# Performance work log

Hardware: AMD Instinct MI355X
Metric: run time of the kernel (lower is better)

Reference implementation:

```python
import jax, jax.numpy as jnp
import numpy as np

N_NODES = 100000
N_EDGES = 1600000
HIDDEN = 128
EF_DIM = 16
LAYERS = 2
N_GRAPHS = 64


def _residual(x, W, b):
    # Residual(mlp_num=2): x + act(act(x@W0+b0)@W1+b1), act = silu
    h = jax.nn.silu(x @ W[0] + b[0])
    h = jax.nn.silu(h @ W[1] + b[1])
    return x + h


def setup_inputs() -> dict:
    key = jax.random.key(0)
    ks = jax.random.split(key, 10)
    scalar = jax.random.normal(ks[0], (N_NODES, HIDDEN), jnp.float32)
    ef = jax.random.normal(ks[1], (N_EDGES, EF_DIM), jnp.float32)
    edge_index = jax.random.randint(ks[2], (2, N_EDGES), 0, N_NODES, jnp.int32)
    C = jax.random.uniform(ks[3], (N_NODES, 1), dtype=jnp.float32)
    conv_smooth = jax.random.uniform(ks[4], (N_EDGES, 1), dtype=jnp.float32)
    batch_index = jnp.sort(jax.random.randint(ks[5], (N_NODES,), 0, N_GRAPHS, jnp.int32))
    # per VD_Conv layer: emb0, emb1, conv0, conv1, out0, out1 residual blocks; + 3 pooling blocks
    n_res = LAYERS * 6 + 3
    res_W = jax.random.normal(ks[6], (n_res, 2, HIDDEN, HIDDEN), jnp.float32) * 0.02
    res_b = jnp.zeros((n_res, 2, HIDDEN), jnp.float32)
    e_lin = jax.random.normal(ks[7], (LAYERS, EF_DIM, HIDDEN), jnp.float32) * 0.02
    return {"scalar": scalar, "ef": ef, "edge_index": edge_index, "C": C,
            "conv_smooth": conv_smooth, "batch_index": batch_index,
            "res_W": res_W, "res_b": res_b, "e_lin": e_lin}


def reference(scalar, ef, edge_index, C, conv_smooth, batch_index, res_W, res_b, e_lin):
    row, col = edge_index[0], edge_index[1]
    for i in range(LAYERS):
        p = 6 * i
        s_src = _residual(scalar, res_W[p], res_b[p])
        s_dst = _residual(scalar, res_W[p + 1], res_b[p + 1])
        conv_filter = (ef @ e_lin[i]) * conv_smooth            # [E, H]
        scalar_edge = s_dst[col] * conv_filter                 # gather + elementwise filter
        conv = jax.ops.segment_sum(scalar_edge, row, num_segments=N_NODES) * C  # scatter-reduce (agg='sum')
        conv = _residual(_residual(conv, res_W[p + 2], res_b[p + 2]), res_W[p + 3], res_b[p + 3])
        s = s_src * conv
        s = _residual(_residual(s, res_W[p + 4], res_b[p + 4]), res_W[p + 5], res_b[p + 5])
        scalar = s + scalar                                    # outer residual in Vanilla_DisGNN
    graph = jax.ops.segment_sum(scalar, batch_index, num_segments=N_GRAPHS)
    q = 6 * LAYERS
    for j in range(3):
        graph = _residual(graph, res_W[q + j], res_b[q + j])
    return graph
```

## Files before the change

### kernel.cpp

```cpp
#include <hip/hip_runtime.h>
#include <hip/hip_bf16.h>
#include <cstdint>
#include <cstddef>

#define HD 128
#define WOFF 32768

typedef __bf16    bf16x8 __attribute__((ext_vector_type(8)));
typedef float     f32x4  __attribute__((ext_vector_type(4)));
typedef _Float16  h2     __attribute__((ext_vector_type(2)));
typedef _Float16  h8     __attribute__((ext_vector_type(8)));

#if defined(__has_builtin)
#if __has_builtin(__builtin_amdgcn_fdot2)
#define HAVE_FDOT2 1
#endif
#endif

__device__ __forceinline__ float fdot2f(h2 a, h2 b, float c) {
#ifdef HAVE_FDOT2
    return __builtin_amdgcn_fdot2(a, b, c, false);
#else
    return c + (float)a[0]*(float)b[0] + (float)a[1]*(float)b[1];
#endif
}

__device__ __forceinline__ int swz(int r, int byteInRow) {
    int chunk = (byteInRow >> 4) ^ (r & 7);
    return r * 256 + (chunk << 4) + (byteInRow & 15);
}

__device__ __forceinline__ float silu_f(float v) { return v / (1.f + __expf(-v)); }


__device__ __forceinline__ void stage_x64(const float* __restrict__ x, char* lds,
                                          int r0, int nrows, int tid) {
    const int q = tid & 15;
    #pragma unroll
    for (int rr = 0; rr < 2; ++rr) {
        const int r  = (tid >> 4) + rr * 32;
        const int gr = r0 + r;
        float4 a = {0,0,0,0}, b = {0,0,0,0};
        if (gr < nrows) {
            const float4* p = (const float4*)(x + (size_t)gr * HD + q * 8);
            a = p[0]; b = p[1];
        }
        bf16x8 v;
        v[0]=(__bf16)a.x; v[1]=(__bf16)a.y; v[2]=(__bf16)a.z; v[3]=(__bf16)a.w;
        v[4]=(__bf16)b.x; v[5]=(__bf16)b.y; v[6]=(__bf16)b.z; v[7]=(__bf16)b.w;
        *(bf16x8*)(lds + swz(r, q * 16)) = v;
    }
}

__device__ __forceinline__ void load_wpref(const __bf16* __restrict__ w, bf16x8 pref[4], int tid) {
    #pragma unroll
    for (int i = 0; i < 4; ++i)
        pref[i] = *(const bf16x8*)(w + (size_t)(i * 512 + tid) * 8);
}
__device__ __forceinline__ void store_wpref(char* lds, const bf16x8 pref[4], int tid) {
    #pragma unroll
    for (int i = 0; i < 4; ++i) {
        const int l = i * 512 + tid;
        *(bf16x8*)(lds + WOFF + swz(l >> 4, (l & 15) * 16)) = pref[i];
    }
}

__device__ __forceinline__ void mm_pass_lds(const char* lds, int src_off,
                                            const float* __restrict__ bias,
                                            int mrow0, int nbase, int crow, int kgrp, f32x4 acc[4]) {
    bf16x8 afr[4];
    #pragma unroll
    for (int kk = 0; kk < 4; ++kk)
        afr[kk] = *(const bf16x8*)(lds + src_off + swz(mrow0 + crow, kk*64 + kgrp*16));
    #pragma unroll
    for (int ni = 0; ni < 4; ++ni) {
        const float bv = bias[(nbase + ni) * 16 + crow];
        f32x4 t = {bv, bv, bv, bv};
        acc[ni] = t;
    }
    #pragma unroll
    for (int ni = 0; ni < 4; ++ni) {
        #pragma unroll
        for (int kk = 0; kk < 4; ++kk) {
            const bf16x8 bfr = *(const bf16x8*)(lds + WOFF + swz((nbase+ni)*16 + crow, kk*64 + kgrp*16));
            acc[ni] = __builtin_amdgcn_mfma_f32_16x16x32_bf16(afr[kk], bfr, acc[ni], 0, 0, 0);
        }
    }
}

__device__ __forceinline__ void write_h64(char* lds, int off, const f32x4 acc[4],
                                          int mrow0, int nbase, int crow, int kgrp) {
    #pragma unroll
    for (int ni = 0; ni < 4; ++ni)
        #pragma unroll
        for (int rg = 0; rg < 4; ++rg)
            *(__bf16*)(lds + off + swz(mrow0 + kgrp*4 + rg, ((nbase+ni)*16 + crow)*2)) =
                (__bf16)silu_f(acc[ni][rg]);
}

__device__ __forceinline__ void restage64(char* lds, const f32x4 carry[4],
                                          int mrow0, int nbase, int crow, int kgrp) {
    #pragma unroll
    for (int ni = 0; ni < 4; ++ni)
        #pragma unroll
        for (int rg = 0; rg < 4; ++rg)
            *(__bf16*)(lds + swz(mrow0 + kgrp*4 + rg, ((nbase+ni)*16 + crow)*2)) =
                (__bf16)carry[ni][rg];
}

__device__ __forceinline__ void sb_pass1(char* lds, const __bf16* __restrict__ w1next,
                                         const float* __restrict__ bias,
                                         int tid, int mrow0, int nbase, int crow, int kgrp, f32x4 acc[4]) {
    bf16x8 pref[4];
    load_wpref(w1next, pref, tid);
    mm_pass_lds(lds, 0, bias, mrow0, nbase, crow, kgrp, acc);
    write_h64(lds, 16384, acc, mrow0, nbase, crow, kgrp);
    __syncthreads();
    store_wpref(lds, pref, tid);
    __syncthreads();
}

__device__ __forceinline__ void bounce_store(const char* lds, int off, __bf16* __restrict__ out,
                                             int r0, int nrows, int tid) {
    const int q = tid & 15;
    #pragma unroll
    for (int rr = 0; rr < 2; ++rr) {
        const int r = (tid >> 4) + rr * 32, gr = r0 + r;
        if (gr < nrows)
            *(bf16x8*)(out + (size_t)gr * HD + q * 8) = *(const bf16x8*)(lds + off + swz(r, q * 16));
    }
}

__global__ __launch_bounds__(512) void resid_dual_kernel(
    const float* __restrict__ x,
    const __bf16* __restrict__ wtA, const float* __restrict__ bA,
    const __bf16* __restrict__ wtB, const float* __restrict__ bB,
    __bf16* __restrict__ out1, __bf16* __restrict__ out2, int nrows)
{
    __shared__ char lds[65536];
    const int tid = threadIdx.x, lane = tid & 63, wv = tid >> 6;
    const int crow = lane & 15, kgrp = lane >> 4;
    const int r0 = blockIdx.x * 64;
    const int mrow0 = (wv >> 1) * 16, nbase = (wv & 1) * 4;

    {
        bf16x8 pref[4];
        load_wpref(wtA, pref, tid);
        stage_x64(x, lds, r0, nrows, tid);
        store_wpref(lds, pref, tid);
    }
    f32x4 acc[4], xe[4];
    #pragma unroll
    for (int ni = 0; ni < 4; ++ni)
        #pragma unroll
        for (int rg = 0; rg < 4; ++rg) {
            const int gr = r0 + mrow0 + kgrp*4 + rg;
            xe[ni][rg] = (gr < nrows) ? x[(size_t)gr*HD + (nbase+ni)*16 + crow] : 0.f;
        }
    __syncthreads();

    sb_pass1(lds, wtA + 16384, bA, tid, mrow0, nbase, crow, kgrp, acc);
    {
        bf16x8 pref[4];
        load_wpref(wtB, pref, tid);
        mm_pass_lds(lds, 16384, bA + HD, mrow0, nbase, crow, kgrp, acc);
        #pragma unroll
        for (int ni = 0; ni < 4; ++ni)
            #pragma unroll
            for (int rg = 0; rg < 4; ++rg)
                *(__bf16*)(lds + 16384 + swz(mrow0 + kgrp*4 + rg, ((nbase+ni)*16 + crow)*2)) =
                    (__bf16)(xe[ni][rg] + silu_f(acc[ni][rg]));
        __syncthreads();
        store_wpref(lds, pref, tid);
        __syncthreads();
    }
    bounce_store(lds, 16384, out1, r0, nrows, tid);
    __syncthreads();

    sb_pass1(lds, wtB + 16384, bB, tid, mrow0, nbase, crow, kgrp, acc);
    mm_pass_lds(lds, 16384, bB + HD, mrow0, nbase, crow, kgrp, acc);
    #pragma unroll
    for (int ni = 0; ni < 4; ++ni)
        #pragma unroll
        for (int rg = 0; rg < 4; ++rg)
            *(__bf16*)(lds + swz(mrow0 + kgrp*4 + rg, ((nbase+ni)*16 + crow)*2)) =
                (__bf16)(xe[ni][rg] + silu_f(acc[ni][rg]));
    __syncthreads();
    bounce_store(lds, 0, out2, r0, nrows, tid);
}

__global__ __launch_bounds__(512) void chain4_kernel(
    const float* __restrict__ x, const __bf16* __restrict__ mid,
    const __bf16* __restrict__ wA, const float* __restrict__ bA,
    const __bf16* __restrict__ wB, const float* __restrict__ bB,
    const __bf16* __restrict__ wC, const float* __restrict__ bC,
    const __bf16* __restrict__ wD, const float* __restrict__ bD,
    const float* __restrict__ post, float* __restrict__ y, int nrows)
{
    __shared__ char lds[65536];
    const int tid = threadIdx.x, lane = tid & 63, wv = tid >> 6;
    const int crow = lane & 15, kgrp = lane >> 4;
    const int r0 = blockIdx.x * 64;
    const int mrow0 = (wv >> 1) * 16, nbase = (wv & 1) * 4;

    {
        bf16x8 pref[4];
        load_wpref(wA, pref, tid);
        stage_x64(x, lds, r0, nrows, tid);
        store_wpref(lds, pref, tid);
    }
    f32x4 carry[4], acc[4];
    #pragma unroll
    for (int ni = 0; ni < 4; ++ni)
        #pragma unroll
        for (int rg = 0; rg < 4; ++rg) {
            const int gr = r0 + mrow0 + kgrp*4 + rg;
            carry[ni][rg] = (gr < nrows) ? x[(size_t)gr*HD + (nbase+ni)*16 + crow] : 0.f;
        }
    __syncthreads();

    sb_pass1(lds, wA + 16384, bA, tid, mrow0, nbase, crow, kgrp, acc);
    {
        bf16x8 pref[4];
        load_wpref(wB, pref, tid);
        mm_pass_lds(lds, 16384, bA + HD, mrow0, nbase, crow, kgrp, acc);
        #pragma unroll
        for (int ni = 0; ni < 4; ++ni)
            #pragma unroll
            for (int rg = 0; rg < 4; ++rg) carry[ni][rg] += silu_f(acc[ni][rg]);
        __syncthreads();
        store_wpref(lds, pref, tid);
        restage64(lds, carry, mrow0, nbase, crow, kgrp);
        __syncthreads();
    }
    sb_pass1(lds, wB + 16384, bB, tid, mrow0, nbase, crow, kgrp, acc);
    {
        bf16x8 pref[4];
        load_wpref(wC, pref, tid);
        mm_pass_lds(lds, 16384, bB + HD, mrow0, nbase, crow, kgrp, acc);
        #pragma unroll
        for (int ni = 0; ni < 4; ++ni)
            #pragma unroll
            for (int rg = 0; rg < 4; ++rg) {
                const int gr = r0 + mrow0 + kgrp*4 + rg;
                const float m = (gr < nrows) ? (float)mid[(size_t)gr*HD + (nbase+ni)*16 + crow] : 0.f;
                carry[ni][rg] = (carry[ni][rg] + silu_f(acc[ni][rg])) * m;
            }
        __syncthreads();
        store_wpref(lds, pref, tid);
        restage64(lds, carry, mrow0, nbase, crow, kgrp);
        __syncthreads();
    }
    sb_pass1(lds, wC + 16384, bC, tid, mrow0, nbase, crow, kgrp, acc);
    {
        bf16x8 pref[4];
        load_wpref(wD, pref, tid);
        mm_pass_lds(lds, 16384, bC + HD, mrow0, nbase, crow, kgrp, acc);
        #pragma unroll
        for (int ni = 0; ni < 4; ++ni)
            #pragma unroll
            for (int rg = 0; rg < 4; ++rg) carry[ni][rg] += silu_f(acc[ni][rg]);
        __syncthreads();
        store_wpref(lds, pref, tid);
        restage64(lds, carry, mrow0, nbase, crow, kgrp);
        __syncthreads();
    }
    sb_pass1(lds, wD + 16384, bD, tid, mrow0, nbase, crow, kgrp, acc);
    mm_pass_lds(lds, 16384, bD + HD, mrow0, nbase, crow, kgrp, acc);
    #pragma unroll
    for (int ni = 0; ni < 4; ++ni)
        #pragma unroll
        for (int rg = 0; rg < 4; ++rg) {
            const int gr = r0 + mrow0 + kgrp*4 + rg;
            if (gr < nrows) {
                const int cc = (nbase+ni)*16 + crow;
                y[(size_t)gr*HD + cc] = carry[ni][rg] + silu_f(acc[ni][rg]) + post[(size_t)gr*HD + cc];
            }
        }
}

__global__ __launch_bounds__(512) void chain3_kernel(
    const float* __restrict__ x,
    const __bf16* __restrict__ wA, const float* __restrict__ bA,
    const __bf16* __restrict__ wB, const float* __restrict__ bB,
    const __bf16* __restrict__ wC, const float* __restrict__ bC,
    float* __restrict__ y, int nrows)
{
    __shared__ char lds[65536];
    const int tid = threadIdx.x, lane = tid & 63, wv = tid >> 6;
    const int crow = lane & 15, kgrp = lane >> 4;
    const int r0 = blockIdx.x * 64;
    const int mrow0 = (wv >> 1) * 16, nbase = (wv & 1) * 4;

    {
        bf16x8 pref[4];
        load_wpref(wA, pref, tid);
        stage_x64(x, lds, r0, nrows, tid);
        store_wpref(lds, pref, tid);
    }
    f32x4 carry[4], acc[4];
    #pragma unroll
    for (int ni = 0; ni < 4; ++ni)
        #pragma unroll
        for (int rg = 0; rg < 4; ++rg) {
            const int gr = r0 + mrow0 + kgrp*4 + rg;
            carry[ni][rg] = (gr < nrows) ? x[(size_t)gr*HD + (nbase+ni)*16 + crow] : 0.f;
        }
    __syncthreads();

    sb_pass1(lds, wA + 16384, bA, tid, mrow0, nbase, crow, kgrp, acc);
    {
        bf16x8 pref[4];
        load_wpref(wB, pref, tid);
        mm_pass_lds(lds, 16384, bA + HD, mrow0, nbase, crow, kgrp, acc);
        #pragma unroll
        for (int ni = 0; ni < 4; ++ni)
            #pragma unroll
            for (int rg = 0; rg < 4; ++rg) carry[ni][rg] += silu_f(acc[ni][rg]);
        __syncthreads();
        store_wpref(lds, pref, tid);
        restage64(lds, carry, mrow0, nbase, crow, kgrp);
        __syncthreads();
    }
    sb_pass1(lds, wB + 16384, bB, tid, mrow0, nbase, crow, kgrp, acc);
    {
        bf16x8 pref[4];
        load_wpref(wC, pref, tid);
        mm_pass_lds(lds, 16384, bB + HD, mrow0, nbase, crow, kgrp, acc);
        #pragma unroll
        for (int ni = 0; ni < 4; ++ni)
            #pragma unroll
            for (int rg = 0; rg < 4; ++rg) carry[ni][rg] += silu_f(acc[ni][rg]);
        __syncthreads();
        store_wpref(lds, pref, tid);
        restage64(lds, carry, mrow0, nbase, crow, kgrp);
        __syncthreads();
    }
    sb_pass1(lds, wC + 16384, bC, tid, mrow0, nbase, crow, kgrp, acc);
    mm_pass_lds(lds, 16384, bC + HD, mrow0, nbase, crow, kgrp, acc);
    #pragma unroll
    for (int ni = 0; ni < 4; ++ni)
        #pragma unroll
        for (int rg = 0; rg < 4; ++rg) {
            const int gr = r0 + mrow0 + kgrp*4 + rg;
            if (gr < nrows)
                y[(size_t)gr*HD + (nbase+ni)*16 + crow] = carry[ni][rg] + silu_f(acc[ni][rg]);
        }
}

__global__ __launch_bounds__(256) void hist_kernel(const int* __restrict__ erow, int* __restrict__ cnt, int E) {
    int i = blockIdx.x * blockDim.x + threadIdx.x;
    const int stride = gridDim.x * blockDim.x;
    for (; i < E; i += stride) atomicAdd(&cnt[erow[i]], 1);
}

__global__ __launch_bounds__(256) void scan1_kernel(const int* __restrict__ cnt, int* __restrict__ part, int n) {
    __shared__ int red[256];
    const int base = blockIdx.x * 1024;
    int s = 0;
    for (int i = threadIdx.x; i < 1024; i += 256) {
        const int idx = base + i;
        s += (idx < n) ? cnt[idx] : 0;
    }
    red[threadIdx.x] = s; __syncthreads();
    for (int o = 128; o > 0; o >>= 1) {
        if (threadIdx.x < o) red[threadIdx.x] += red[threadIdx.x + o];
        __syncthreads();
    }
    if (threadIdx.x == 0) part[blockIdx.x] = red[0];
}

__global__ __launch_bounds__(256) void scan2_kernel(int* __restrict__ part, int nb,
                                                    int* __restrict__ rowptr, int n) {
    __shared__ int sh[257];
    const int tid = threadIdx.x;
    int a[4]; int s = 0;
    #pragma unroll
    for (int q = 0; q < 4; ++q) {
        const int i = tid*4 + q;
        a[q] = (i < nb) ? part[i] : 0;
        s += a[q];
    }
    sh[tid + 1] = s; __syncthreads();
    if (tid == 0) {
        sh[0] = 0;
        int run = 0;
        for (int i = 1; i <= 256; ++i) { run += sh[i]; sh[i] = run; }
    }
    __syncthreads();
    int off = sh[tid];
    #pragma unroll
    for (int q = 0; q < 4; ++q) {
        const int i = tid*4 + q;
        if (i < nb) part[i] = off;
        off += a[q];
    }
    if (tid == 255) rowptr[n] = off;
}

__global__ __launch_bounds__(256) void scan3_kernel(const int* __restrict__ cnt, const int* __restrict__ part,
                                                    int* __restrict__ rowptr, int n) {
    __shared__ int sc[257];
    const int base = blockIdx.x * 1024;
    const int i0 = base + threadIdx.x * 4;
    int v[4]; int s = 0;
    #pragma unroll
    for (int q = 0; q < 4; ++q) {
        const int idx = i0 + q;
        v[q] = (idx < n) ? cnt[idx] : 0;
        s += v[q];
    }
    sc[threadIdx.x + 1] = s; __syncthreads();
    if (threadIdx.x == 0) {
        int run = 0;
        for (int i = 0; i < 256; ++i) { const int t = sc[i + 1]; sc[i + 1] = run; run += t; }
    }
    __syncthreads();
    int off = part[blockIdx.x] + sc[threadIdx.x + 1];
    #pragma unroll
    for (int q = 0; q < 4; ++q) {
        const int idx = i0 + q;
        if (idx < n) rowptr[idx] = off;
        off += v[q];
    }
}

__global__ __launch_bounds__(256) void scatter_reorder_kernel(
    const int* __restrict__ erow, const int* __restrict__ ecol,
    const float* __restrict__ ef, const float* __restrict__ cs,
    const int* __restrict__ rowptr, int* __restrict__ cursor,
    int* __restrict__ csr_col, _Float16* __restrict__ csr_ef, int E)
{
    int i = blockIdx.x * blockDim.x + threadIdx.x;
    const int stride = gridDim.x * blockDim.x;
    for (; i < E; i += stride) {
        const int r = erow[i];
        const int p = rowptr[r] + atomicAdd(&cursor[r], 1);
        csr_col[p] = ecol[i];
        const float c = cs[i];
        const float4* ep = (const float4*)(ef + (size_t)i * 16);
        const float4 e0 = ep[0], e1 = ep[1], e2 = ep[2], e3 = ep[3];
        h8 v0, v1;
        v0[0]=(_Float16)(e0.x*c); v0[1]=(_Float16)(e0.y*c); v0[2]=(_Float16)(e0.z*c); v0[3]=(_Float16)(e0.w*c);
        v0[4]=(_Float16)(e1.x*c); v0[5]=(_Float16)(e1.y*c); v0[6]=(_Float16)(e1.z*c); v0[7]=(_Float16)(e1.w*c);
        v1[0]=(_Float16)(e2.x*c); v1[1]=(_Float16)(e2.y*c); v1[2]=(_Float16)(e2.z*c); v1[3]=(_Float16)(e2.w*c);
        v1[4]=(_Float16)(e3.x*c); v1[5]=(_Float16)(e3.y*c); v1[6]=(_Float16)(e3.z*c); v1[7]=(_Float16)(e3.w*c);
        h8* dst = (h8*)(csr_ef + (size_t)p * 16);
        dst[0] = v0; dst[1] = v1;
    }
}

__global__ __launch_bounds__(256) void elin16_kernel(const float* __restrict__ elin,
                                                     _Float16* __restrict__ out, int total) {
    const int i = blockIdx.x * 256 + threadIdx.x;
    if (i < total) out[i] = (_Float16)elin[i];
}

__device__ __forceinline__ float bfu_lo(uint32_t u) { return __uint_as_float(u << 16); }
__device__ __forceinline__ float bfu_hi(uint32_t u) { return __uint_as_float(u & 0xffff0000u); }

__device__ __forceinline__ void edge_dot(const h8 a0, const h8 a1,
                                         const h2 w0[8], const h2 w1[8],
                                         float& f0, float& f1) {
    #pragma unroll
    for (int kk = 0; kk < 4; ++kk) {
        h2 p = {a0[2*kk], a0[2*kk+1]};
        f0 = fdot2f(p, w0[kk], f0);
        f1 = fdot2f(p, w1[kk], f1);
    }
    #pragma unroll
    for (int kk = 0; kk < 4; ++kk) {
        h2 p = {a1[2*kk], a1[2*kk+1]};
        f0 = fdot2f(p, w0[4+kk], f0);
        f1 = fdot2f(p, w1[4+kk], f1);
    }
}

__global__ __launch_bounds__(256) void conv_kernel(
    const _Float16* __restrict__ csr_ef, const int* __restrict__ csr_col,
    const _Float16* __restrict__ elin16, const int* __restrict__ rowptr,
    const __bf16* __restrict__ sdst, const float* __restrict__ Cn,
    float* __restrict__ conv, int nnodes)
{
    const int wv   = __builtin_amdgcn_readfirstlane(threadIdx.x >> 6);
    const int lane = threadIdx.x & 63;
    const int v = blockIdx.x * 4 + wv;
    if (v >= nnodes) return;
    const int j0 = lane * 2;

    h2 w0[8], w1[8];
    #pragma unroll
    for (int kk = 0; kk < 8; ++kk) {
        w0[kk][0] = elin16[(2*kk)   * HD + j0];
        w0[kk][1] = elin16[(2*kk+1) * HD + j0];
        w1[kk][0] = elin16[(2*kk)   * HD + j0 + 1];
        w1[kk][1] = elin16[(2*kk+1) * HD + j0 + 1];
    }

    const uint16_t* sd = (const uint16_t*)sdst;
    const int beg = rowptr[v], end = rowptr[v + 1];
    float acc0 = 0.f, acc1 = 0.f;
    int t = beg;
    for (; t + 4 <= end; t += 4) {
        int c[4];
        #pragma unroll
        for (int q = 0; q < 4; ++q) c[q] = csr_col[t + q];
        uint32_t u[4];
        #pragma unroll
        for (int q = 0; q < 4; ++q)
            u[q] = *(const uint32_t*)(sd + (size_t)c[q] * HD + j0);
        #pragma unroll
        for (int q = 0; q < 4; ++q) {
            const h8* ep = (const h8*)(csr_ef + (size_t)(t + q) * 16);
            const h8 a0 = ep[0], a1 = ep[1];
            float f0 = 0.f, f1 = 0.f;
            edge_dot(a0, a1, w0, w1, f0, f1);
            acc0 = fmaf(bfu_lo(u[q]), f0, acc0);
            acc1 = fmaf(bfu_hi(u[q]), f1, acc1);
        }
    }
    for (; t < end; ++t) {
        const int c = csr_col[t];
        const uint32_t u = *(const uint32_t*)(sd + (size_t)c * HD + j0);
        const h8* ep = (const h8*)(csr_ef + (size_t)t * 16);
        const h8 a0 = ep[0], a1 = ep[1];
        float f0 = 0.f, f1 = 0.f;
        edge_dot(a0, a1, w0, w1, f0, f1);
        acc0 = fmaf(bfu_lo(u), f0, acc0);
        acc1 = fmaf(bfu_hi(u), f1, acc1);
    }
    const float cn = Cn[v];
    float2 out = {acc0 * cn, acc1 * cn};
    *(float2*)(conv + (size_t)v * HD + j0) = out;
}

__global__ __launch_bounds__(256) void pool_kernel(
    const float* __restrict__ s, const int* __restrict__ bidx,
    float* __restrict__ g, int n)
{
    const int slot = threadIdx.x >> 5;
    const int jc   = (threadIdx.x & 31) * 4;
    const int base = blockIdx.x * 256;
    if (base >= n) return;
    const int end = (base + 256 < n) ? base + 256 : n;
    float4 acc = {0,0,0,0};
    int cur = -1;
    for (int i = base + slot; i < end; i += 8) {
        const int b = bidx[i];
        if (b != cur) {
            if (cur >= 0) {
                atomicAdd(g + (size_t)cur*HD + jc + 0, acc.x);
                atomicAdd(g + (size_t)cur*HD + jc + 1, acc.y);
                atomicAdd(g + (size_t)cur*HD + jc + 2, acc.z);
                atomicAdd(g + (size_t)cur*HD + jc + 3, acc.w);
            }
            acc = {0,0,0,0};
            cur = b;
        }
        const float4 v = *(const float4*)(s + (size_t)i*HD + jc);
        acc.x += v.x; acc.y += v.y; acc.z += v.z; acc.w += v.w;
    }
    if (cur >= 0) {
        atomicAdd(g + (size_t)cur*HD + jc + 0, acc.x);
        atomicAdd(g + (size_t)cur*HD + jc + 1, acc.y);
        atomicAdd(g + (size_t)cur*HD + jc + 2, acc.z);
        atomicAdd(g + (size_t)cur*HD + jc + 3, acc.w);
    }
}

__global__ __launch_bounds__(256) void convw_kernel(const float* __restrict__ W, __bf16* __restrict__ wt, int total) {
    const int idx = blockIdx.x * 256 + threadIdx.x;
    if (idx >= total) return;
    const int mat = idx >> 14;
    const int rem = idx & 16383;
    const int jj = rem >> 7, kk = rem & 127;
    wt[idx] = (__bf16)W[(size_t)mat * 16384 + kk * HD + jj];
}

extern "C" void kernel_launch(void* const* d_in, const int* in_sizes, int n_in,
                              void* d_out, int out_size, void* d_ws, size_t ws_size,
                              hipStream_t stream) {
    const float* scalar = (const float*)d_in[0];
    const float* ef     = (const float*)d_in[1];
    const int*   eidx   = (const int*)  d_in[2];
    const float* Cn     = (const float*)d_in[3];
    const float* cs     = (const float*)d_in[4];
    const int*   bidx   = (const int*)  d_in[5];
    const float* resW   = (const float*)d_in[6];
    const float* resB   = (const float*)d_in[7];
    const float* elin   = (const float*)d_in[8];

    const int N      = in_sizes[0] / HD;
    const int E      = in_sizes[1] / 16;
    const int n_res  = in_sizes[7] / (2 * HD);
    const int layers = (n_res - 3) / 6;
    const int G      = out_size / HD;
    const size_t nfeat = (size_t)N * HD;

    char* p = (char*)d_ws;
    auto alloc = [&](size_t bytes) { char* q = p; p += (bytes + 255) & ~(size_t)255; return q; };
    float*    A      = (float*)alloc(nfeat * 4);
    float*    Dc     = (float*)alloc(nfeat * 4);
    __bf16*   Bs16   = (__bf16*)alloc(nfeat * 2);
    __bf16*   Cs16   = (__bf16*)alloc(nfeat * 2);
    __bf16*   wt     = (__bf16*)alloc((size_t)n_res * 2 * 16384 * 2);
    float*    graph  = (float*)alloc((size_t)G * HD * 4);
    int*      rowptr = (int*)alloc((size_t)(N + 1) * 4);
    int*      rowcnt = (int*)alloc((size_t)N * 4);
    int*      csr_col= (int*)alloc((size_t)E * 4);
    _Float16* csr_ef = (_Float16*)alloc((size_t)E * 16 * 2);
    _Float16* elin16 = (_Float16*)alloc((size_t)layers * 16 * HD * 2);
    int*      part   = (int*)alloc(1024 * 4);

    const int* erow = eidx;
    const int* ecol = eidx + E;

    const int totW = n_res * 2 * 16384;
    convw_kernel<<<(totW + 255) / 256, 256, 0, stream>>>(resW, wt, totW);
    const int totE = layers * 16 * HD;
    elin16_kernel<<<(totE + 255) / 256, 256, 0, stream>>>(elin, elin16, totE);

    const int nchunks = (N + 1023) / 1024;
    hipMemsetAsync(rowcnt, 0, (size_t)N * 4, stream);
    hist_kernel<<<1024, 256, 0, stream>>>(erow, rowcnt, E);
    scan1_kernel<<<nchunks, 256, 0, stream>>>(rowcnt, part, N);
    scan2_kernel<<<1, 256, 0, stream>>>(part, nchunks, rowptr, N);
    scan3_kernel<<<nchunks, 256, 0, stream>>>(rowcnt, part, rowptr, N);
    hipMemsetAsync(rowcnt, 0, (size_t)N * 4, stream);
    scatter_reorder_kernel<<<1024, 256, 0, stream>>>(erow, ecol, ef, cs, rowptr, rowcnt, csr_col, csr_ef, E);

    const int gridR = (N + 63) / 64;
    const float* cur = scalar;
    for (int i = 0; i < layers; ++i) {
        const int pb = 6 * i;
        resid_dual_kernel<<<gridR, 512, 0, stream>>>(
            cur,
            wt + (size_t)pb * 32768, resB + (size_t)pb * 256,
            wt + (size_t)(pb + 1) * 32768, resB + (size_t)(pb + 1) * 256,
            Bs16, Cs16, N);
        conv_kernel<<<(N + 3) / 4, 256, 0, stream>>>(
            csr_ef, csr_col, elin16 + (size_t)i * 16 * HD, rowptr, Cs16, Cn, Dc, N);
        chain4_kernel<<<gridR, 512, 0, stream>>>(
            Dc, Bs16,
            wt + (size_t)(pb + 2) * 32768, resB + (size_t)(pb + 2) * 256,
            wt + (size_t)(pb + 3) * 32768, resB + (size_t)(pb + 3) * 256,
            wt + (size_t)(pb + 4) * 32768, resB + (size_t)(pb + 4) * 256,
            wt + (size_t)(pb + 5) * 32768, resB + (size_t)(pb + 5) * 256,
            cur, A, N);
        cur = A;
    }

    hipMemsetAsync(graph, 0, (size_t)G * HD * 4, stream);
    pool_kernel<<<(N + 255) / 256, 256, 0, stream>>>(cur, bidx, graph, N);

    const int q = 6 * layers;
    const int gridG = (G + 63) / 64;
    chain3_kernel<<<gridG, 512, 0, stream>>>(
        graph,
        wt + (size_t)q * 32768, resB + (size_t)q * 256,
        wt + (size_t)(q + 1) * 32768, resB + (size_t)(q + 1) * 256,
        wt + (size_t)(q + 2) * 32768, resB + (size_t)(q + 2) * 256,
        (float*)d_out, G);
}
```

Before: 886.5 us.

## Shrink LDS to 48KB with in-place activation staging and wider edge unroll

The fused residual MLP kernels now overwrite the activation tile in place instead of ping-ponging between two 16KB regions. An extra barrier after each matmul read makes that overwrite safe. This moves the weight region to offset 16384 and cuts shared memory from 64KB to 48KB per block, which may allow more resident blocks per CU. resid_dual also writes its outputs straight from registers as scattered bf16 stores instead of bouncing them through LDS. Separately, the CSR gather loop is unrolled to 8 edges with a 2-edge remainder loop to keep more loads in flight, at the cost of more registers.

```diff
diff --git a/kernel.cpp b/kernel.cpp
--- a/kernel.cpp
+++ b/kernel.cpp
@@ -4,7 +4,7 @@
 #include <cstddef>
 
 #define HD 128
-#define WOFF 32768
+#define WOFF 16384
 
 typedef __bf16    bf16x8 __attribute__((ext_vector_type(8)));
 typedef float     f32x4  __attribute__((ext_vector_type(4)));
@@ -65,13 +65,13 @@
     }
 }
 
-__device__ __forceinline__ void mm_pass_lds(const char* lds, int src_off,
+__device__ __forceinline__ void mm_pass_lds(const char* lds,
                                             const float* __restrict__ bias,
                                             int mrow0, int nbase, int crow, int kgrp, f32x4 acc[4]) {
     bf16x8 afr[4];
     #pragma unroll
     for (int kk = 0; kk < 4; ++kk)
-        afr[kk] = *(const bf16x8*)(lds + src_off + swz(mrow0 + crow, kk*64 + kgrp*16));
+        afr[kk] = *(const bf16x8*)(lds + swz(mrow0 + crow, kk*64 + kgrp*16));
     #pragma unroll
     for (int ni = 0; ni < 4; ++ni) {
         const float bv = bias[(nbase + ni) * 16 + crow];
@@ -88,13 +88,13 @@
     }
 }
 
-__device__ __forceinline__ void write_h64(char* lds, int off, const f32x4 acc[4],
+__device__ __forceinline__ void write_h64(char* lds, const f32x4 acc[4],
                                           int mrow0, int nbase, int crow, int kgrp) {
     #pragma unroll
     for (int ni = 0; ni < 4; ++ni)
         #pragma unroll
         for (int rg = 0; rg < 4; ++rg)
-            *(__bf16*)(lds + off + swz(mrow0 + kgrp*4 + rg, ((nbase+ni)*16 + crow)*2)) =
+            *(__bf16*)(lds + swz(mrow0 + kgrp*4 + rg, ((nbase+ni)*16 + crow)*2)) =
                 (__bf16)silu_f(acc[ni][rg]);
 }
 
@@ -106,29 +106,6 @@
         for (int rg = 0; rg < 4; ++rg)
             *(__bf16*)(lds + swz(mrow0 + kgrp*4 + rg, ((nbase+ni)*16 + crow)*2)) =
                 (__bf16)carry[ni][rg];
-}
-
-__device__ __forceinline__ void sb_pass1(char* lds, const __bf16* __restrict__ w1next,
-                                         const float* __restrict__ bias,
-                                         int tid, int mrow0, int nbase, int crow, int kgrp, f32x4 acc[4]) {
-    bf16x8 pref[4];
-    load_wpref(w1next, pref, tid);
-    mm_pass_lds(lds, 0, bias, mrow0, nbase, crow, kgrp, acc);
-    write_h64(lds, 16384, acc, mrow0, nbase, crow, kgrp);
-    __syncthreads();
-    store_wpref(lds, pref, tid);
-    __syncthreads();
-}
-
-__device__ __forceinline__ void bounce_store(const char* lds, int off, __bf16* __restrict__ out,
-                                             int r0, int nrows, int tid) {
-    const int q = tid & 15;
-    #pragma unroll
-    for (int rr = 0; rr < 2; ++rr) {
-        const int r = (tid >> 4) + rr * 32, gr = r0 + r;
-        if (gr < nrows)
-            *(bf16x8*)(out + (size_t)gr * HD + q * 8) = *(const bf16x8*)(lds + off + swz(r, q * 16));
-    }
 }
 
 __global__ __launch_bounds__(512) void resid_dual_kernel(
@@ -137,7 +114,7 @@
     const __bf16* __restrict__ wtB, const float* __restrict__ bB,
     __bf16* __restrict__ out1, __bf16* __restrict__ out2, int nrows)
 {
-    __shared__ char lds[65536];
+    __shared__ char lds[49152];
     const int tid = threadIdx.x, lane = tid & 63, wv = tid >> 6;
     const int crow = lane & 15, kgrp = lane >> 4;
     const int r0 = blockIdx.x * 64;
@@ -159,34 +136,81 @@
         }
     __syncthreads();
 
-    sb_pass1(lds, wtA + 16384, bA, tid, mrow0, nbase, crow, kgrp, acc);
+    {
+        bf16x8 pref[4];
+        load_wpref(wtA + 16384, pref, tid);
+        mm_pass_lds(lds, bA, mrow0, nbase, crow, kgrp, acc);
+        __syncthreads();
+        write_h64(lds, acc, mrow0, nbase, crow, kgrp);
+        store_wpref(lds, pref, tid);
+        __syncthreads();
+    }
     {
         bf16x8 pref[4];
         load_wpref(wtB, pref, tid);
-        mm_pass_lds(lds, 16384, bA + HD, mrow0, nbase, crow, kgrp, acc);
+        mm_pass_lds(lds, bA + HD, mrow0, nbase, crow, kgrp, acc);
         #pragma unroll
         for (int ni = 0; ni < 4; ++ni)
             #pragma unroll
-            for (int rg = 0; rg < 4; ++rg)
-                *(__bf16*)(lds + 16384 + swz(mrow0 + kgrp*4 + rg, ((nbase+ni)*16 + crow)*2)) =
+            for (int rg = 0; rg < 4; ++rg) {
+                const int gr = r0 + mrow0 + kgrp*4 + rg;
+                if (gr < nrows)
+                    out1[(size_t)gr*HD + (nbase+ni)*16 + crow] =
+                        (__bf16)(xe[ni][rg] + silu_f(acc[ni][rg]));
+            }
+        __syncthreads();
+        restage64(lds, xe, mrow0, nbase, crow, kgrp);
+        store_wpref(lds, pref, tid);
+        __syncthreads();
+    }
+    {
+        bf16x8 pref[4];
+        load_wpref(wtB + 16384, pref, tid);
+        mm_pass_lds(lds, bB, mrow0, nbase, crow, kgrp, acc);
+        __syncthreads();
+        write_h64(lds, acc, mrow0, nbase, crow, kgrp);
+        store_wpref(lds, pref, tid);
+        __syncthreads();
+    }
+    mm_pass_lds(lds, bB + HD, mrow0, nbase, crow, kgrp, acc);
+    #pragma unroll
+    for (int ni = 0; ni < 4; ++ni)
+        #pragma unroll
+        for (int rg = 0; rg < 4; ++rg) {
+            const int gr = r0 + mrow0 + kgrp*4 + rg;
+            if (gr < nrows)
+                out2[(size_t)gr*HD + (nbase+ni)*16 + crow] =
                     (__bf16)(xe[ni][rg] + silu_f(acc[ni][rg]));
-        __syncthreads();
-        store_wpref(lds, pref, tid);
-        __syncthreads();
-    }
-    bounce_store(lds, 16384, out1, r0, nrows, tid);
-    __syncthreads();
-
-    sb_pass1(lds, wtB + 16384, bB, tid, mrow0, nbase, crow, kgrp, acc);
-    mm_pass_lds(lds, 16384, bB + HD, mrow0, nbase, crow, kgrp, acc);
-    #pragma unroll
-    for (int ni = 0; ni < 4; ++ni)
-        #pragma unroll
-        for (int rg = 0; rg < 4; ++rg)
-            *(__bf16*)(lds + swz(mrow0 + kgrp*4 + rg, ((nbase+ni)*16 + crow)*2)) =
-                (__bf16)(xe[ni][rg] + silu_f(acc[ni][rg]));
-    __syncthreads();
-    bounce_store(lds, 0, out2, r0, nrows, tid);
+        }
+}
+
+__device__ __forceinline__ void sub_block(char* lds, const __bf16* __restrict__ w1,
+                                          const __bf16* __restrict__ wNext0,
+                                          const float* __restrict__ bias,
+                                          int tid, int mrow0, int nbase, int crow, int kgrp,
+                                          f32x4 carry[4], f32x4 acc[4]) {
+    {
+        bf16x8 pref[4];
+        load_wpref(w1, pref, tid);
+        mm_pass_lds(lds, bias, mrow0, nbase, crow, kgrp, acc);
+        __syncthreads();
+        write_h64(lds, acc, mrow0, nbase, crow, kgrp);
+        store_wpref(lds, pref, tid);
+        __syncthreads();
+    }
+    {
+        bf16x8 pref[4];
+        load_wpref(wNext0, pref, tid);
+        mm_pass_lds(lds, bias + HD, mrow0, nbase, crow, kgrp, acc);
+        #pragma unroll
+        for (int ni = 0; ni < 4; ++ni)
+            #pragma unroll
+            for (int rg = 0; rg < 4; ++rg) carry[ni][rg] += silu_f(acc[ni][rg]);
+        __syncthreads();
+        restage64(lds, carry, mrow0, nbase, crow, kgrp);
+        store_wpref(lds, pref, tid);
+        __syncthreads();
+    }
 }
 
 __global__ __launch_bounds__(512) void chain4_kernel(
@@ -197,7 +221,7 @@
     const __bf16* __restrict__ wD, const float* __restrict__ bD,
     const float* __restrict__ post, float* __restrict__ y, int nrows)
 {
-    __shared__ char lds[65536];
+    __shared__ char lds[49152];
     const int tid = threadIdx.x, lane = tid & 63, wv = tid >> 6;
     const int crow = lane & 15, kgrp = lane >> 4;
     const int r0 = blockIdx.x * 64;
@@ -219,25 +243,20 @@
         }
     __syncthreads();
 
-    sb_pass1(lds, wA + 16384, bA, tid, mrow0, nbase, crow, kgrp, acc);
-    {
-        bf16x8 pref[4];
-        load_wpref(wB, pref, tid);
-        mm_pass_lds(lds, 16384, bA + HD, mrow0, nbase, crow, kgrp, acc);
-        #pragma unroll
-        for (int ni = 0; ni < 4; ++ni)
-            #pragma unroll
-            for (int rg = 0; rg < 4; ++rg) carry[ni][rg] += silu_f(acc[ni][rg]);
-        __syncthreads();
-        store_wpref(lds, pref, tid);
-        restage64(lds, carry, mrow0, nbase, crow, kgrp);
-        __syncthreads();
-    }
-    sb_pass1(lds, wB + 16384, bB, tid, mrow0, nbase, crow, kgrp, acc);
+    sub_block(lds, wA + 16384, wB, bA, tid, mrow0, nbase, crow, kgrp, carry, acc);
+    {
+        bf16x8 pref[4];
+        load_wpref(wB + 16384, pref, tid);
+        mm_pass_lds(lds, bB, mrow0, nbase, crow, kgrp, acc);
+        __syncthreads();
+        write_h64(lds, acc, mrow0, nbase, crow, kgrp);
+        store_wpref(lds, pref, tid);
+        __syncthreads();
+    }
     {
         bf16x8 pref[4];
         load_wpref(wC, pref, tid);
-        mm_pass_lds(lds, 16384, bB + HD, mrow0, nbase, crow, kgrp, acc);
+        mm_pass_lds(lds, bB + HD, mrow0, nbase, crow, kgrp, acc);
         #pragma unroll
         for (int ni = 0; ni < 4; ++ni)
             #pragma unroll
@@ -247,26 +266,21 @@
                 carry[ni][rg] = (carry[ni][rg] + silu_f(acc[ni][rg])) * m;
             }
         __syncthreads();
-        store_wpref(lds, pref, tid);
         restage64(lds, carry, mrow0, nbase, crow, kgrp);
-        __syncthreads();
-    }
-    sb_pass1(lds, wC + 16384, bC, tid, mrow0, nbase, crow, kgrp, acc);
-    {
-        bf16x8 pref[4];
-        load_wpref(wD, pref, tid);
-        mm_pass_lds(lds, 16384, bC + HD, mrow0, nbase, crow, kgrp, acc);
-        #pragma unroll
-        for (int ni = 0; ni < 4; ++ni)
-            #pragma unroll
-            for (int rg = 0; rg < 4; ++rg) carry[ni][rg] += silu_f(acc[ni][rg]);
-        __syncthreads();
-        store_wpref(lds, pref, tid);
-        restage64(lds, carry, mrow0, nbase, crow, kgrp);
-        __syncthreads();
-    }
-    sb_pass1(lds, wD + 16384, bD, tid, mrow0, nbase, crow, kgrp, acc);
-    mm_pass_lds(lds, 16384, bD + HD, mrow0, nbase, crow, kgrp, acc);
+        store_wpref(lds, pref, tid);
+        __syncthreads();
+    }
+    sub_block(lds, wC + 16384, wD, bC, tid, mrow0, nbase, crow, kgrp, carry, acc);
+    {
+        bf16x8 pref[4];
+        load_wpref(wD + 16384, pref, tid);
+        mm_pass_lds(lds, bD, mrow0, nbase, crow, kgrp, acc);
+        __syncthreads();
+        write_h64(lds, acc, mrow0, nbase, crow, kgrp);
+        store_wpref(lds, pref, tid);
+        __syncthreads();
+    }
+    mm_pass_lds(lds, bD + HD, mrow0, nbase, crow, kgrp, acc);
     #pragma unroll
     for (int ni = 0; ni < 4; ++ni)
         #pragma unroll
@@ -286,7 +300,7 @@
     const __bf16* __restrict__ wC, const float* __restrict__ bC,
     float* __restrict__ y, int nrows)
 {
-    __shared__ char lds[65536];
+    __shared__ char lds[49152];
     const int tid = threadIdx.x, lane = tid & 63, wv = tid >> 6;
     const int crow = lane & 15, kgrp = lane >> 4;
     const int r0 = blockIdx.x * 64;
@@ -308,36 +322,18 @@
         }
     __syncthreads();
 
-    sb_pass1(lds, wA + 16384, bA, tid, mrow0, nbase, crow, kgrp, acc);
-    {
-        bf16x8 pref[4];
-        load_wpref(wB, pref, tid);
-        mm_pass_lds(lds, 16384, bA + HD, mrow0, nbase, crow, kgrp, acc);
-        #pragma unroll
-        for (int ni = 0; ni < 4; ++ni)
-            #pragma unroll
-            for (int rg = 0; rg < 4; ++rg) carry[ni][rg] += silu_f(acc[ni][rg]);
-        __syncthreads();
-        store_wpref(lds, pref, tid);
-        restage64(lds, carry, mrow0, nbase, crow, kgrp);
-        __syncthreads();
-    }
-    sb_pass1(lds, wB + 16384, bB, tid, mrow0, nbase, crow, kgrp, acc);
-    {
-        bf16x8 pref[4];
-        load_wpref(wC, pref, tid);
-        mm_pass_lds(lds, 16384, bB + HD, mrow0, nbase, crow, kgrp, acc);
-        #pragma unroll
-        for (int ni = 0; ni < 4; ++ni)
-            #pragma unroll
-            for (int rg = 0; rg < 4; ++rg) carry[ni][rg] += silu_f(acc[ni][rg]);
-        __syncthreads();
-        store_wpref(lds, pref, tid);
-        restage64(lds, carry, mrow0, nbase, crow, kgrp);
-        __syncthreads();
-    }
-    sb_pass1(lds, wC + 16384, bC, tid, mrow0, nbase, crow, kgrp, acc);
-    mm_pass_lds(lds, 16384, bC + HD, mrow0, nbase, crow, kgrp, acc);
+    sub_block(lds, wA + 16384, wB, bA, tid, mrow0, nbase, crow, kgrp, carry, acc);
+    sub_block(lds, wB + 16384, wC, bB, tid, mrow0, nbase, crow, kgrp, carry, acc);
+    {
+        bf16x8 pref[4];
+        load_wpref(wC + 16384, pref, tid);
+        mm_pass_lds(lds, bC, mrow0, nbase, crow, kgrp, acc);
+        __syncthreads();
+        write_h64(lds, acc, mrow0, nbase, crow, kgrp);
+        store_wpref(lds, pref, tid);
+        __syncthreads();
+    }
+    mm_pass_lds(lds, bC + HD, mrow0, nbase, crow, kgrp, acc);
     #pragma unroll
     for (int ni = 0; ni < 4; ++ni)
         #pragma unroll
@@ -501,16 +497,16 @@
     const int beg = rowptr[v], end = rowptr[v + 1];
     float acc0 = 0.f, acc1 = 0.f;
     int t = beg;
-    for (; t + 4 <= end; t += 4) {
-        int c[4];
-        #pragma unroll
-        for (int q = 0; q < 4; ++q) c[q] = csr_col[t + q];
-        uint32_t u[4];
-        #pragma unroll
-        for (int q = 0; q < 4; ++q)
+    for (; t + 8 <= end; t += 8) {
+        int c[8];
+        #pragma unroll
+        for (int q = 0; q < 8; ++q) c[q] = csr_col[t + q];
+        uint32_t u[8];
+        #pragma unroll
+        for (int q = 0; q < 8; ++q)
             u[q] = *(const uint32_t*)(sd + (size_t)c[q] * HD + j0);
         #pragma unroll
-        for (int q = 0; q < 4; ++q) {
+        for (int q = 0; q < 8; ++q) {
             const h8* ep = (const h8*)(csr_ef + (size_t)(t + q) * 16);
             const h8 a0 = ep[0], a1 = ep[1];
             float f0 = 0.f, f1 = 0.f;
@@ -519,7 +515,23 @@
             acc1 = fmaf(bfu_hi(u[q]), f1, acc1);
         }
     }
-    for (; t < end; ++t) {
+    for (; t + 2 <= end; t += 2) {
+        int c[2];
+        c[0] = csr_col[t]; c[1] = csr_col[t + 1];
+        uint32_t u[2];
+        u[0] = *(const uint32_t*)(sd + (size_t)c[0] * HD + j0);
+        u[1] = *(const uint32_t*)(sd + (size_t)c[1] * HD + j0);
+        #pragma unroll
+        for (int q = 0; q < 2; ++q) {
+            const h8* ep = (const h8*)(csr_ef + (size_t)(t + q) * 16);
+            const h8 a0 = ep[0], a1 = ep[1];
+            float f0 = 0.f, f1 = 0.f;
+            edge_dot(a0, a1, w0, w1, f0, f1);
+            acc0 = fmaf(bfu_lo(u[q]), f0, acc0);
+            acc1 = fmaf(bfu_hi(u[q]), f1, acc1);
+        }
+    }
+    if (t < end) {
         const int c = csr_col[t];
         const uint32_t u = *(const uint32_t*)(sd + (size_t)c * HD + j0);
         const h8* ep = (const h8*)(csr_ef + (size_t)t * 16);
```

Result: faster. 840.9 us (-5.1%).
